# Kernel optimization log

Hardware: AMD Instinct MI355X
Metric: run time of the kernel (lower is better)

Reference implementation:

```python
import jax, jax.numpy as jnp
import numpy as np

ALPHA = 0.2
SIGMA_REC = 0.15

def setup_inputs() -> dict:
    key = jax.random.key(0)
    k1, k2, k3, k4, k5 = jax.random.split(key, 5)
    B, T, n, d_in = 256, 2048, 64, 6
    u = jax.random.normal(k1, (B, T, d_in), dtype=jnp.float32)
    noise = jax.random.normal(k2, (B, T, n), dtype=jnp.float32)
    # scale recurrent weight down so the 2048-step unroll stays numerically stable
    W_rec = jax.random.normal(k3, (n, n), dtype=jnp.float32) * 0.1
    W_in = jax.random.normal(k4, (n, d_in), dtype=jnp.float32)
    W_out = jax.random.normal(k5, (2, n), dtype=jnp.float32)
    return {"u": u, "noise": noise, "W_rec": W_rec, "W_in": W_in, "W_out": W_out}

def reference(u, noise, W_rec, W_in, W_out):
    B, T, _ = u.shape
    n = W_rec.shape[0]
    alpha = jnp.float32(ALPHA)
    noise_scale = jnp.sqrt(2.0 * alpha * jnp.float32(SIGMA_REC) ** 2)
    nz = noise_scale * noise  # [B, T, n]

    # Precompute the input drive for all steps: u @ W_in.T -> [B, T, n]
    drive = jnp.einsum('btd,nd->btn', u, W_in) + nz

    def step(s, d_t):
        # s: [B, n]; d_t: [B, n] = W_in u_t + noise_t
        s_new = (1.0 - alpha) * s + alpha * jax.nn.relu(s @ W_rec.T + d_t)
        return s_new, s_new

    s0 = jnp.zeros((B, n), dtype=u.dtype)
    # loop runs t-1 steps (original: for i in range(t-1)), using drive[:, :-1]
    _, ss = jax.lax.scan(step, s0, jnp.swapaxes(drive[:, :-1, :], 0, 1))  # [T-1, B, n]
    states = jnp.concatenate([s0[:, None, :], jnp.swapaxes(ss, 0, 1)], axis=1)  # [B, T, n]
    out = jnp.einsum('btn,on->bto', states, W_out)  # [B, T, 2]
    return states, out
```

## Files before the change

kernel.cpp:

```cpp
#include <hip/hip_runtime.h>
#include <hip/hip_bf16.h>

#define BATCH 256
#define TSTEPS 2048
#define NDIM 64
#define DIN 6
#define ALPHA 0.2f
#define NSCALE 0.09486832980505137f

__device__ __forceinline__ float rdlane(float v, int lane) {
    return __uint_as_float((unsigned)__builtin_amdgcn_readlane((int)__float_as_uint(v), lane));
}

__global__ __launch_bounds__(64, 1) void rnn_scan_kernel(
    const float* __restrict__ u,
    const float* __restrict__ noise,
    const float* __restrict__ W_rec,
    const float* __restrict__ W_in,
    float* __restrict__ states)
{
    const int b = blockIdx.x;
    const int j = threadIdx.x;

    float4 w4[16];
    const float4* wr = reinterpret_cast<const float4*>(W_rec + j * NDIM);
#pragma unroll
    for (int i = 0; i < 16; ++i) w4[i] = wr[i];

    float win[DIN];
#pragma unroll
    for (int d = 0; d < DIN; ++d) win[d] = W_in[j * DIN + d];

    const float* nb = noise + (size_t)b * TSTEPS * NDIM;
    const float4* ub4 = reinterpret_cast<const float4*>(u + (size_t)b * TSTEPS * DIN);
    float* st = states + (size_t)b * TSTEPS * NDIM;

    float s = 0.0f;
    st[j] = 0.0f;

    auto step_body = [&](int t, float nvk, const float* uuf) {
        float ax = 0.0f, ay = 0.0f, az = 0.0f, aw = 0.0f;
#pragma unroll
        for (int i = 0; i < 16; ++i) {
            const float4 wv = w4[i];
            const float sx = rdlane(s, 4 * i + 0);
            const float sy = rdlane(s, 4 * i + 1);
            const float sz = rdlane(s, 4 * i + 2);
            const float sw = rdlane(s, 4 * i + 3);
            ax = fmaf(wv.x, sx, ax);
            ay = fmaf(wv.y, sy, ay);
            az = fmaf(wv.z, sz, az);
            aw = fmaf(wv.w, sw, aw);
        }
        float d = NSCALE * nvk;
#pragma unroll
        for (int kk = 0; kk < DIN; ++kk) d = fmaf(win[kk], uuf[kk], d);

        const float acc = ((ax + ay) + (az + aw)) + d;
        s = fmaf(1.0f - ALPHA, s, ALPHA * fmaxf(acc, 0.0f));

        st[(size_t)(t + 1) * NDIM + j] = s;
    };

    float nva[8], nvb[8];
    float4 uua[12], uub[12];
#pragma unroll
    for (int k = 0; k < 8; ++k) nva[k] = nb[k * NDIM + j];
#pragma unroll
    for (int k = 0; k < 12; ++k) uua[k] = ub4[k];

    auto run8 = [&](int tb, const float* nv, const float4* uu,
                    float* nvN, float4* uuN) {
        const int tpf = tb + 8;
#pragma unroll
        for (int k = 0; k < 8; ++k) nvN[k] = nb[(tpf + k) * NDIM + j];
        const int ubase = tpf * DIN / 4;
#pragma unroll
        for (int k = 0; k < 12; ++k) uuN[k] = ub4[ubase + k];

        const float* uuf = reinterpret_cast<const float*>(uu);
#pragma unroll
        for (int k = 0; k < 8; ++k) step_body(tb + k, nv[k], uuf + k * DIN);
    };

    int tb = 0;
    for (int it = 0; it < 127; ++it) {
        run8(tb, nva, uua, nvb, uub); tb += 8;
        run8(tb, nvb, uub, nva, uua); tb += 8;
    }
    run8(2032, nva, uua, nvb, uub);
    {
        const float* uuf = reinterpret_cast<const float*>(uub);
#pragma unroll
        for (int k = 0; k < 7; ++k) step_body(2040 + k, nvb[k], uuf + k * DIN);
    }
}

__global__ __launch_bounds__(256) void out_proj_kernel(
    const float* __restrict__ states,
    const float* __restrict__ W_out,
    float* __restrict__ out)
{
    const int lane = threadIdx.x & 63;
    const int seg = lane & 3;
    const int rsub = lane >> 2;

    const size_t wave = (size_t)(blockIdx.x * blockDim.x + threadIdx.x) >> 6;
    const size_t nwaves = ((size_t)gridDim.x * blockDim.x) >> 6;
    const size_t ngroups = (size_t)BATCH * TSTEPS / 16;

    float4 w0[4], w1[4];
    const float4* wo = reinterpret_cast<const float4*>(W_out);
#pragma unroll
    for (int i = 0; i < 4; ++i) {
        w0[i] = wo[seg * 4 + i];
        w1[i] = wo[16 + seg * 4 + i];
    }

    for (size_t g = wave; g < ngroups; g += nwaves) {
        const size_t r = g * 16 + rsub;
        const float4* sp = reinterpret_cast<const float4*>(states + r * NDIM + seg * 16);
        float p0 = 0.0f, p1 = 0.0f;
#pragma unroll
        for (int i = 0; i < 4; ++i) {
            const float4 sv = sp[i];
            p0 = fmaf(sv.x, w0[i].x, p0); p0 = fmaf(sv.y, w0[i].y, p0);
            p0 = fmaf(sv.z, w0[i].z, p0); p0 = fmaf(sv.w, w0[i].w, p0);
            p1 = fmaf(sv.x, w1[i].x, p1); p1 = fmaf(sv.y, w1[i].y, p1);
            p1 = fmaf(sv.z, w1[i].z, p1); p1 = fmaf(sv.w, w1[i].w, p1);
        }
        p0 += __shfl_xor(p0, 1); p0 += __shfl_xor(p0, 2);
        p1 += __shfl_xor(p1, 1); p1 += __shfl_xor(p1, 2);
        if (seg == 0) {
            reinterpret_cast<float2*>(out)[r] = make_float2(p0, p1);
        }
    }
}

extern "C" void kernel_launch(void* const* d_in, const int* in_sizes, int n_in,
                              void* d_out, int out_size, void* d_ws, size_t ws_size,
                              hipStream_t stream) {
    const float* u     = (const float*)d_in[0];
    const float* noise = (const float*)d_in[1];
    const float* W_rec = (const float*)d_in[2];
    const float* W_in  = (const float*)d_in[3];
    const float* W_out = (const float*)d_in[4];

    float* states = (float*)d_out;
    float* out    = states + (size_t)BATCH * TSTEPS * NDIM;

    rnn_scan_kernel<<<BATCH, 64, 0, stream>>>(u, noise, W_rec, W_in, states);
    out_proj_kernel<<<2048, 256, 0, stream>>>(states, W_out, out);
}
```

Before: 698.5 us.

## Split recurrent matvec across four waves and fuse output projection into scan

Each batch block now runs four waves, and each wave computes a quarter of the 64-term recurrent dot product. The partial sums are combined through double-buffered LDS with a workgroup barrier every timestep. The output projection is folded into the scan: two waves reduce W_out·s with cross-lane shuffles, which removes the second kernel and its re-read of all states. The cost is a barrier plus LDS traffic on the serial critical path of every step.

```diff
diff --git a/kernel.cpp b/kernel.cpp
--- a/kernel.cpp
+++ b/kernel.cpp
@@ -1,5 +1,4 @@
 #include <hip/hip_runtime.h>
-#include <hip/hip_bf16.h>
 
 #define BATCH 256
 #define TSTEPS 2048
@@ -12,54 +11,80 @@
     return __uint_as_float((unsigned)__builtin_amdgcn_readlane((int)__float_as_uint(v), lane));
 }
 
-__global__ __launch_bounds__(64, 1) void rnn_scan_kernel(
+__global__ __launch_bounds__(256, 1) void rnn_fused_kernel(
     const float* __restrict__ u,
     const float* __restrict__ noise,
     const float* __restrict__ W_rec,
     const float* __restrict__ W_in,
-    float* __restrict__ states)
+    const float* __restrict__ W_out,
+    float* __restrict__ states,
+    float* __restrict__ out)
 {
     const int b = blockIdx.x;
-    const int j = threadIdx.x;
+    const int tid = threadIdx.x;
+    const int w = tid >> 6;
+    const int j = tid & 63;
 
-    float4 w4[16];
-    const float4* wr = reinterpret_cast<const float4*>(W_rec + j * NDIM);
+    __shared__ float part[2][4][NDIM];
+
+    float wc[16];
 #pragma unroll
-    for (int i = 0; i < 16; ++i) w4[i] = wr[i];
+    for (int k = 0; k < 16; ++k) wc[k] = W_rec[j * NDIM + 4 * k + w];
 
     float win[DIN];
 #pragma unroll
     for (int d = 0; d < DIN; ++d) win[d] = W_in[j * DIN + d];
 
+    float wo = 0.0f;
+    if (w == 1) wo = W_out[j];
+    else if (w == 2) wo = W_out[NDIM + j];
+
     const float* nb = noise + (size_t)b * TSTEPS * NDIM;
     const float4* ub4 = reinterpret_cast<const float4*>(u + (size_t)b * TSTEPS * DIN);
     float* st = states + (size_t)b * TSTEPS * NDIM;
+    float* ob = out + (size_t)b * TSTEPS * 2;
 
     float s = 0.0f;
-    st[j] = 0.0f;
+    if (w == 0) st[j] = 0.0f;
+    if ((w == 1 || w == 2) && j == 0) ob[w - 1] = 0.0f;
 
-    auto step_body = [&](int t, float nvk, const float* uuf) {
-        float ax = 0.0f, ay = 0.0f, az = 0.0f, aw = 0.0f;
+    int p = 0;
+    float prb[8];
+
+    auto step_body = [&](int t, float nvk, const float* uuf, int k8) {
+        float a = 0.0f;
 #pragma unroll
-        for (int i = 0; i < 16; ++i) {
-            const float4 wv = w4[i];
-            const float sx = rdlane(s, 4 * i + 0);
-            const float sy = rdlane(s, 4 * i + 1);
-            const float sz = rdlane(s, 4 * i + 2);
-            const float sw = rdlane(s, 4 * i + 3);
-            ax = fmaf(wv.x, sx, ax);
-            ay = fmaf(wv.y, sy, ay);
-            az = fmaf(wv.z, sz, az);
-            aw = fmaf(wv.w, sw, aw);
+        for (int k = 0; k < 16; ++k) {
+            a = fmaf(wc[k], rdlane(s, 4 * k + w), a);
         }
         float d = NSCALE * nvk;
 #pragma unroll
         for (int kk = 0; kk < DIN; ++kk) d = fmaf(win[kk], uuf[kk], d);
 
-        const float acc = ((ax + ay) + (az + aw)) + d;
+        part[p][w][j] = a;
+        asm volatile("s_waitcnt lgkmcnt(0)" ::: "memory");
+        __builtin_amdgcn_s_barrier();
+        asm volatile("" ::: "memory");
+        const float a0 = part[p][0][j];
+        const float a1 = part[p][1][j];
+        const float a2 = part[p][2][j];
+        const float a3 = part[p][3][j];
+        const float acc = ((a0 + a1) + (a2 + a3)) + d;
         s = fmaf(1.0f - ALPHA, s, ALPHA * fmaxf(acc, 0.0f));
+        p ^= 1;
 
-        st[(size_t)(t + 1) * NDIM + j] = s;
+        if (w == 0) {
+            st[(size_t)(t + 1) * NDIM + j] = s;
+        } else if (w == 1 || w == 2) {
+            float pr = wo * s;
+            pr += __shfl_xor(pr, 1);
+            pr += __shfl_xor(pr, 2);
+            pr += __shfl_xor(pr, 4);
+            pr += __shfl_xor(pr, 8);
+            pr += __shfl_xor(pr, 16);
+            pr += __shfl_xor(pr, 32);
+            prb[k8] = pr;
+        }
     };
 
     float nva[8], nvb[8];
@@ -80,7 +105,13 @@
 
         const float* uuf = reinterpret_cast<const float*>(uu);
 #pragma unroll
-        for (int k = 0; k < 8; ++k) step_body(tb + k, nv[k], uuf + k * DIN);
+        for (int k = 0; k < 8; ++k) step_body(tb + k, nv[k], uuf + k * DIN, k);
+
+        if ((w == 1 || w == 2) && j == 0) {
+#pragma unroll
+            for (int k = 0; k < 8; ++k)
+                ob[(size_t)(tb + 1 + k) * 2 + (w - 1)] = prb[k];
+        }
     };
 
     int tb = 0;
@@ -92,47 +123,11 @@
     {
         const float* uuf = reinterpret_cast<const float*>(uub);
 #pragma unroll
-        for (int k = 0; k < 7; ++k) step_body(2040 + k, nvb[k], uuf + k * DIN);
-    }
-}
-
-__global__ __launch_bounds__(256) void out_proj_kernel(
-    const float* __restrict__ states,
-    const float* __restrict__ W_out,
-    float* __restrict__ out)
-{
-    const int lane = threadIdx.x & 63;
-    const int seg = lane & 3;
-    const int rsub = lane >> 2;
-
-    const size_t wave = (size_t)(blockIdx.x * blockDim.x + threadIdx.x) >> 6;
-    const size_t nwaves = ((size_t)gridDim.x * blockDim.x) >> 6;
-    const size_t ngroups = (size_t)BATCH * TSTEPS / 16;
-
-    float4 w0[4], w1[4];
-    const float4* wo = reinterpret_cast<const float4*>(W_out);
+        for (int k = 0; k < 7; ++k) step_body(2040 + k, nvb[k], uuf + k * DIN, k);
+        if ((w == 1 || w == 2) && j == 0) {
 #pragma unroll
-    for (int i = 0; i < 4; ++i) {
-        w0[i] = wo[seg * 4 + i];
-        w1[i] = wo[16 + seg * 4 + i];
-    }
-
-    for (size_t g = wave; g < ngroups; g += nwaves) {
-        const size_t r = g * 16 + rsub;
-        const float4* sp = reinterpret_cast<const float4*>(states + r * NDIM + seg * 16);
-        float p0 = 0.0f, p1 = 0.0f;
-#pragma unroll
-        for (int i = 0; i < 4; ++i) {
-            const float4 sv = sp[i];
-            p0 = fmaf(sv.x, w0[i].x, p0); p0 = fmaf(sv.y, w0[i].y, p0);
-            p0 = fmaf(sv.z, w0[i].z, p0); p0 = fmaf(sv.w, w0[i].w, p0);
-            p1 = fmaf(sv.x, w1[i].x, p1); p1 = fmaf(sv.y, w1[i].y, p1);
-            p1 = fmaf(sv.z, w1[i].z, p1); p1 = fmaf(sv.w, w1[i].w, p1);
-        }
-        p0 += __shfl_xor(p0, 1); p0 += __shfl_xor(p0, 2);
-        p1 += __shfl_xor(p1, 1); p1 += __shfl_xor(p1, 2);
-        if (seg == 0) {
-            reinterpret_cast<float2*>(out)[r] = make_float2(p0, p1);
+            for (int k = 0; k < 7; ++k)
+                ob[(size_t)(2041 + k) * 2 + (w - 1)] = prb[k];
         }
     }
 }
@@ -149,6 +144,6 @@
     float* states = (float*)d_out;
     float* out    = states + (size_t)BATCH * TSTEPS * NDIM;
 
-    rnn_scan_kernel<<<BATCH, 64, 0, stream>>>(u, noise, W_rec, W_in, states);
-    out_proj_kernel<<<2048, 256, 0, stream>>>(states, W_out, out);
+    rnn_fused_kernel<<<BATCH, 256, 0, stream>>>(u, noise, W_rec, W_in, W_out,
+                                                states, out);
 }
```

Result: slower. 1.437 ms (+105.7%).

## Fuse output projection into recurrent scan kernel and pack 8 batches per block

Applied to the files above, without the earlier changes.

Removes the separate output-projection kernel. Each wave now computes the two output channels per step with a cross-lane shuffle reduction right after updating its state, and writes them out in batches of eight steps. The launch also changes from 256 single-wave blocks to 32 blocks of 8 waves. This avoids re-reading the full states tensor from memory and one kernel launch. In exchange it adds shuffle work to every serial recurrence step and concentrates the waves on fewer CUs.

```diff
diff --git a/kernel.cpp b/kernel.cpp
--- a/kernel.cpp
+++ b/kernel.cpp
@@ -1,5 +1,4 @@
 #include <hip/hip_runtime.h>
-#include <hip/hip_bf16.h>
 
 #define BATCH 256
 #define TSTEPS 2048
@@ -12,15 +11,18 @@
     return __uint_as_float((unsigned)__builtin_amdgcn_readlane((int)__float_as_uint(v), lane));
 }
 
-__global__ __launch_bounds__(64, 1) void rnn_scan_kernel(
+__global__ __launch_bounds__(512, 2) void rnn_fused_kernel(
     const float* __restrict__ u,
     const float* __restrict__ noise,
     const float* __restrict__ W_rec,
     const float* __restrict__ W_in,
-    float* __restrict__ states)
+    const float* __restrict__ W_out,
+    float* __restrict__ states,
+    float* __restrict__ out)
 {
-    const int b = blockIdx.x;
-    const int j = threadIdx.x;
+    const int w = threadIdx.x >> 6;
+    const int j = threadIdx.x & 63;
+    const int b = blockIdx.x * 8 + w;
 
     float4 w4[16];
     const float4* wr = reinterpret_cast<const float4*>(W_rec + j * NDIM);
@@ -31,14 +33,21 @@
 #pragma unroll
     for (int d = 0; d < DIN; ++d) win[d] = W_in[j * DIN + d];
 
+    const float wo0 = W_out[j];
+    const float wo1 = W_out[NDIM + j];
+
     const float* nb = noise + (size_t)b * TSTEPS * NDIM;
     const float4* ub4 = reinterpret_cast<const float4*>(u + (size_t)b * TSTEPS * DIN);
     float* st = states + (size_t)b * TSTEPS * NDIM;
+    float* ob = out + (size_t)b * TSTEPS * 2;
 
     float s = 0.0f;
     st[j] = 0.0f;
+    if (j == 0) reinterpret_cast<float2*>(ob)[0] = make_float2(0.0f, 0.0f);
 
-    auto step_body = [&](int t, float nvk, const float* uuf) {
+    float prb[8];
+
+    auto step_body = [&](int t, float nvk, const float* uuf, int k8) {
         float ax = 0.0f, ay = 0.0f, az = 0.0f, aw = 0.0f;
 #pragma unroll
         for (int i = 0; i < 16; ++i) {
@@ -60,6 +69,18 @@
         s = fmaf(1.0f - ALPHA, s, ALPHA * fmaxf(acc, 0.0f));
 
         st[(size_t)(t + 1) * NDIM + j] = s;
+
+        const float q0 = wo0 * s;
+        const float q1 = wo1 * s;
+        const float t0 = __shfl_xor(q0, 32);
+        const float t1 = __shfl_xor(q1, 32);
+        float r = (j & 32) ? (q1 + t1) : (q0 + t0);
+        r += __shfl_xor(r, 1);
+        r += __shfl_xor(r, 2);
+        r += __shfl_xor(r, 4);
+        r += __shfl_xor(r, 8);
+        r += __shfl_xor(r, 16);
+        prb[k8] = r;
     };
 
     float nva[8], nvb[8];
@@ -80,7 +101,14 @@
 
         const float* uuf = reinterpret_cast<const float*>(uu);
 #pragma unroll
-        for (int k = 0; k < 8; ++k) step_body(tb + k, nv[k], uuf + k * DIN);
+        for (int k = 0; k < 8; ++k) step_body(tb + k, nv[k], uuf + k * DIN, k);
+
+        if ((j & 31) == 0) {
+            const int o = j >> 5;
+#pragma unroll
+            for (int k = 0; k < 8; ++k)
+                ob[(size_t)(tb + 1 + k) * 2 + o] = prb[k];
+        }
     };
 
     int tb = 0;
@@ -92,47 +120,12 @@
     {
         const float* uuf = reinterpret_cast<const float*>(uub);
 #pragma unroll
-        for (int k = 0; k < 7; ++k) step_body(2040 + k, nvb[k], uuf + k * DIN);
-    }
-}
-
-__global__ __launch_bounds__(256) void out_proj_kernel(
-    const float* __restrict__ states,
-    const float* __restrict__ W_out,
-    float* __restrict__ out)
-{
-    const int lane = threadIdx.x & 63;
-    const int seg = lane & 3;
-    const int rsub = lane >> 2;
-
-    const size_t wave = (size_t)(blockIdx.x * blockDim.x + threadIdx.x) >> 6;
-    const size_t nwaves = ((size_t)gridDim.x * blockDim.x) >> 6;
-    const size_t ngroups = (size_t)BATCH * TSTEPS / 16;
-
-    float4 w0[4], w1[4];
-    const float4* wo = reinterpret_cast<const float4*>(W_out);
+        for (int k = 0; k < 7; ++k) step_body(2040 + k, nvb[k], uuf + k * DIN, k);
+        if ((j & 31) == 0) {
+            const int o = j >> 5;
 #pragma unroll
-    for (int i = 0; i < 4; ++i) {
-        w0[i] = wo[seg * 4 + i];
-        w1[i] = wo[16 + seg * 4 + i];
-    }
-
-    for (size_t g = wave; g < ngroups; g += nwaves) {
-        const size_t r = g * 16 + rsub;
-        const float4* sp = reinterpret_cast<const float4*>(states + r * NDIM + seg * 16);
-        float p0 = 0.0f, p1 = 0.0f;
-#pragma unroll
-        for (int i = 0; i < 4; ++i) {
-            const float4 sv = sp[i];
-            p0 = fmaf(sv.x, w0[i].x, p0); p0 = fmaf(sv.y, w0[i].y, p0);
-            p0 = fmaf(sv.z, w0[i].z, p0); p0 = fmaf(sv.w, w0[i].w, p0);
-            p1 = fmaf(sv.x, w1[i].x, p1); p1 = fmaf(sv.y, w1[i].y, p1);
-            p1 = fmaf(sv.z, w1[i].z, p1); p1 = fmaf(sv.w, w1[i].w, p1);
-        }
-        p0 += __shfl_xor(p0, 1); p0 += __shfl_xor(p0, 2);
-        p1 += __shfl_xor(p1, 1); p1 += __shfl_xor(p1, 2);
-        if (seg == 0) {
-            reinterpret_cast<float2*>(out)[r] = make_float2(p0, p1);
+            for (int k = 0; k < 7; ++k)
+                ob[(size_t)(2041 + k) * 2 + o] = prb[k];
         }
     }
 }
@@ -149,6 +142,6 @@
     float* states = (float*)d_out;
     float* out    = states + (size_t)BATCH * TSTEPS * NDIM;
 
-    rnn_scan_kernel<<<BATCH, 64, 0, stream>>>(u, noise, W_rec, W_in, states);
-    out_proj_kernel<<<2048, 256, 0, stream>>>(states, W_out, out);
+    rnn_fused_kernel<<<32, 512, 0, stream>>>(u, noise, W_rec, W_in, W_out,
+                                             states, out);
 }
```

New measurement: 1.472 ms. +110.7%, slower.
